# Kernel optimization log

Measured on AMD Instinct MI355X. Metric: run time of the kernel, lower is better.

The kernel has to match this reference:

```python
import jax, jax.numpy as jnp
import numpy as np

N = 100000      # nodes
E = 3200000     # edges (avg degree 32)
F_IN = 500      # input features
HID = 8         # per-head hidden dim (layer 1)
HEADS = 8       # heads (layer 1)
NC = 41         # num classes (layer 2, 1 head)


def setup_inputs() -> dict:
    key = jax.random.key(0)
    ks = jax.random.split(key, 8)
    x = jax.random.normal(ks[0], (N, F_IN), jnp.float32)
    edge_index = jax.random.randint(ks[1], (2, E), 0, N, dtype=jnp.int64)
    W1 = jax.random.normal(ks[2], (F_IN, HEADS * HID), jnp.float32) / np.sqrt(F_IN)
    a1_src = jax.random.normal(ks[3], (HEADS, HID), jnp.float32) / np.sqrt(HID)
    a1_dst = jax.random.normal(ks[4], (HEADS, HID), jnp.float32) / np.sqrt(HID)
    W2 = jax.random.normal(ks[5], (HEADS * HID, NC), jnp.float32) / np.sqrt(HEADS * HID)
    a2_src = jax.random.normal(ks[6], (1, NC), jnp.float32) / np.sqrt(NC)
    a2_dst = jax.random.normal(ks[7], (1, NC), jnp.float32) / np.sqrt(NC)
    return {"x": x, "edge_index": edge_index, "W1": W1, "a1_src": a1_src,
            "a1_dst": a1_dst, "W2": W2, "a2_src": a2_src, "a2_dst": a2_dst}


def gat_layer(x, edge_index, W, a_src, a_dst, heads, out_dim, concat):
    n = x.shape[0]
    h = (x @ W).reshape(n, heads, out_dim)                    # [N,H,D]
    # per-node attention halves (avoids gathering full features for logits)
    alpha_src = jnp.einsum('nhd,hd->nh', h, a_src)            # [N,H]
    alpha_dst = jnp.einsum('nhd,hd->nh', h, a_dst)            # [N,H]
    src, dst = edge_index[0], edge_index[1]
    e = jax.nn.leaky_relu(alpha_src[src] + alpha_dst[dst], 0.2)  # [E,H]
    # segment softmax over incoming edges of each destination node
    e_max = jax.lax.stop_gradient(jax.ops.segment_max(e, dst, num_segments=n))
    e_exp = jnp.exp(e - e_max[dst])
    denom = jax.ops.segment_sum(e_exp, dst, num_segments=n)
    alpha = e_exp / (denom[dst] + 1e-16)                      # [E,H]
    msg = alpha[:, :, None] * h[src]                          # [E,H,D]
    out = jax.ops.segment_sum(msg, dst, num_segments=n)       # [N,H,D]
    return out.reshape(n, heads * out_dim) if concat else out.mean(axis=1)


def reference(x, edge_index, W1, a1_src, a1_dst, W2, a2_src, a2_dst):
    # dropout layers are identity at inference
    h = gat_layer(x, edge_index, W1, a1_src, a1_dst, HEADS, HID, True)   # [N,64]
    h = jax.nn.elu(h)
    out = gat_layer(h, edge_index, W2, a2_src, a2_dst, 1, NC, False)     # [N,41]
    return jax.nn.log_softmax(out, axis=1)
```

## Files before the change

### kernel.cpp

```cpp
#include <hip/hip_runtime.h>
#include <hip/hip_bf16.h>
#include <math.h>


#define DEV __device__ __forceinline__

constexpr int N_NODES = 100000;
constexpr int N_EDGES = 3200000;
constexpr int F_IN    = 500;
constexpr int HEADS   = 8;
constexpr int HID     = 8;
constexpr int D1      = HEADS * HID;
constexpr int NC      = 41;
constexpr int NCP     = 64;

constexpr int NB    = 196;
constexpr int BCAP  = 20480;
constexpr int CSTR  = 16;
constexpr int SEPT  = 8;
constexpr int SCHUNK = 512 * SEPT;
constexpr int SBLKS = (N_EDGES + SCHUNK - 1) / SCHUNK;

constexpr int GROWS = 32;
constexpr int LROW  = 520;
constexpr int GBLKS = N_NODES / GROWS;

constexpr int WSTR = 68;

typedef __attribute__((ext_vector_type(8))) short bf16x8;
typedef __attribute__((ext_vector_type(4))) float f32x4;

DEV float bf2f(unsigned short u) {
    return __uint_as_float(((unsigned int)u) << 16);
}
DEV unsigned short f2b(float f) {
    unsigned int u = __float_as_uint(f);
    unsigned int r = (u + 0x7FFFu + ((u >> 16) & 1u)) >> 16;
    return (unsigned short)r;
}
DEV float leaky(float e) { return e > 0.f ? e : 0.2f * e; }
DEV float readlane_f(float v, int l) {
    return __uint_as_float((unsigned int)__builtin_amdgcn_readlane((int)__float_as_uint(v), l));
}

__global__ void k_detect(const void* xraw, const void* eraw, int* flags) {
    const int lane = threadIdx.x & 63;
    const unsigned short* xu = (const unsigned short*)xraw;
    unsigned short v = xu[2 * lane];
    int e = (v >> 7) & 0xFF;
    int valid = (e == 0 || (e >= 90 && e <= 150)) ? 1 : 0;
    unsigned long long vm = __ballot(valid);
    const unsigned int* eu = (const unsigned int*)eraw;
    unsigned long long zm = __ballot(eu[2 * lane + 1] == 0u);
    if (lane == 0) {
        flags[0] = (__popcll(vm) < 56) ? 1 : 0;
        flags[1] = (__popcll(zm) == 64) ? 1 : 0;
    }
}

__global__ __launch_bounds__(256) void k_convert(const void* w1, const void* a1s, const void* a1d,
                                                 const void* w2, const void* a2s, const void* a2d,
                                                 const int* flags,
                                                 unsigned short* W1frag, float* A1Sf, float* A1Df,
                                                 float* W2f, float* A2Sf, float* A2Df) {
    const bool f32 = flags[0] != 0;
    if (blockIdx.x == 0) {
        auto conv = [&](const void* src, float* dst, int n) {
            if (f32) {
                const float* s = (const float*)src;
                for (int i = threadIdx.x; i < n; i += blockDim.x) dst[i] = s[i];
            } else {
                const unsigned short* s = (const unsigned short*)src;
                for (int i = threadIdx.x; i < n; i += blockDim.x) dst[i] = bf2f(s[i]);
            }
        };
        conv(a1s, A1Sf, HEADS * HID);
        conv(a1d, A1Df, HEADS * HID);
        conv(w2, W2f, D1 * NC);
        conv(a2s, A2Sf, NC);
        conv(a2d, A2Df, NC);
    }
    for (int idx = blockIdx.x * 256 + threadIdx.x; idx < 4 * 16 * 64 * 8; idx += 64 * 256) {
        int wid = idx >> 13, kb = (idx >> 9) & 15, ln = (idx >> 3) & 63, j = idx & 7;
        int k = kb * 32 + (ln >> 4) * 8 + j;
        int n = wid * 16 + (ln & 15);
        unsigned short bits = 0;
        if (k < F_IN) {
            if (f32) bits = f2b(((const float*)w1)[k * D1 + n]);
            else     bits = ((const unsigned short*)w1)[k * D1 + n];
        }
        W1frag[idx] = bits;
    }
}

__global__ __launch_bounds__(512, 8) void k_gemm1_scat(const void* xraw, const void* eraw,
                                                       const int* flags,
                                                       const unsigned short* __restrict__ W1frag,
                                                       const float* A1Sf, const float* A1Df,
                                                       unsigned short* __restrict__ h1b,
                                                       float* __restrict__ as1,
                                                       float* __restrict__ ad1,
                                                       int* bucket_cnt, unsigned int* staging) {
    __shared__ unsigned short ldsx[GROWS * LROW];
    const int t = threadIdx.x;

    if (blockIdx.x < SBLKS) {
        int* bh = (int*)ldsx;
        for (int i = t; i < NB; i += 512) bh[i] = 0;
        __syncthreads();
        const bool e64 = flags[1] != 0;
        const unsigned int* eu = (const unsigned int*)eraw;
        const int e0 = blockIdx.x * SCHUNK;
        int sv[SEPT], dv[SEPT];
#pragma unroll
        for (int k = 0; k < SEPT; k++) {
            int i = e0 + k * 512 + t;
            if (i < N_EDGES) {
                if (e64) { sv[k] = (int)eu[2 * i]; dv[k] = (int)eu[2 * (N_EDGES + i)]; }
                else     { sv[k] = (int)eu[i];     dv[k] = (int)eu[N_EDGES + i]; }
                atomicAdd(&bh[dv[k] >> 9], 1);
            } else dv[k] = -1;
        }
        __syncthreads();
        for (int i = t; i < NB; i += 512) {
            int c = bh[i];
            int base = c ? atomicAdd(&bucket_cnt[i * CSTR], c) : 0;
            bh[i] = i * BCAP + base;
        }
        __syncthreads();
#pragma unroll
        for (int k = 0; k < SEPT; k++) {
            if (dv[k] >= 0) {
                int b = dv[k] >> 9;
                int slot = atomicAdd(&bh[b], 1);
                staging[slot] = (unsigned)sv[k] | ((unsigned)(dv[k] & 511) << 17);
            }
        }
        return;
    }

    const int r0 = (blockIdx.x - SBLKS) * GROWS;
    const bool xf32 = flags[0] != 0;
#pragma unroll 4
    for (int it = 0; it < 8; it++) {
        int s = it * 512 + t;
        int row = s >> 7, c4 = s & 127;
        int row_g = r0 + row;
        ushort4 v = make_ushort4(0, 0, 0, 0);
        if (c4 < 125) {
            if (xf32) {
                float4 f = *(const float4*)((const float*)xraw + (size_t)row_g * F_IN + c4 * 4);
                v = make_ushort4(f2b(f.x), f2b(f.y), f2b(f.z), f2b(f.w));
            } else {
                v = *(const ushort4*)((const unsigned short*)xraw + (size_t)row_g * F_IN + c4 * 4);
            }
        }
        *(ushort4*)(ldsx + row * LROW + c4 * 4) = v;
    }
    __syncthreads();

    const int lane = t & 63;
    const int w = t >> 6;
    const int wid = __builtin_amdgcn_readfirstlane(w & 3);
    const int mb  = __builtin_amdgcn_readfirstlane(w >> 2);
    const int m = lane & 15, q = lane >> 4;
    f32x4 acc = {0.f, 0.f, 0.f, 0.f};
    const unsigned short* wf = W1frag + (size_t)wid * 8192;
    const unsigned short* arow = ldsx + (mb * 16 + m) * LROW + q * 8;
#pragma unroll 4
    for (int kb = 0; kb < 16; kb++) {
        bf16x8 b = *(const bf16x8*)(wf + (kb * 64 + lane) * 8);
        bf16x8 a = *(const bf16x8*)(arow + kb * 32);
        acc = __builtin_amdgcn_mfma_f32_16x16x32_bf16(a, b, acc, 0, 0, 0);
    }
    const int col = wid * 16 + m;
    const float a_s = A1Sf[col], a_d = A1Df[col];
    const int h = 2 * wid + (m >> 3);
#pragma unroll
    for (int reg = 0; reg < 4; reg++) {
        int gr = r0 + mb * 16 + q * 4 + reg;
        float vacc = acc[reg];
        h1b[(size_t)gr * D1 + col] = f2b(vacc);
        float ts = vacc * a_s, td = vacc * a_d;
        ts += __shfl_xor(ts, 1, 64); td += __shfl_xor(td, 1, 64);
        ts += __shfl_xor(ts, 2, 64); td += __shfl_xor(td, 2, 64);
        ts += __shfl_xor(ts, 4, 64); td += __shfl_xor(td, 4, 64);
        if ((lane & 7) == 0) {
            as1[gr * HEADS + h] = ts;
            ad1[gr * HEADS + h] = td;
        }
    }
}

__global__ void k_cscan(const int* bucket_cnt, int* cbase, int* off) {
    __shared__ int s[256];
    int t = threadIdx.x;
    s[t] = (t < NB) ? bucket_cnt[t * CSTR] : 0;
    __syncthreads();
    for (int o = 1; o < 256; o <<= 1) {
        int v = (t >= o) ? s[t - o] : 0;
        __syncthreads();
        s[t] += v;
        __syncthreads();
    }
    if (t < NB) cbase[t + 1] = s[t];
    if (t == 0) { cbase[0] = 0; off[N_NODES] = N_EDGES; }
}

__global__ __launch_bounds__(512) void k_csr_build(const unsigned int* __restrict__ staging,
                                                   const int* __restrict__ bucket_cnt,
                                                   const int* __restrict__ cbase,
                                                   int* __restrict__ off, int* __restrict__ csr) {
    __shared__ int sdeg[512];
    __shared__ int scur[512];
    const int t = threadIdx.x;
    const int b = blockIdx.x;
    const int n0 = b << 9;
    const int start = b * BCAP;
    const int end = start + bucket_cnt[b * CSTR];
    const int base = cbase[b];
    sdeg[t] = 0;
    __syncthreads();
    for (int i = start + t; i < end; i += 512)
        atomicAdd(&sdeg[staging[i] >> 17], 1);
    __syncthreads();
    int d = sdeg[t];
    for (int o = 1; o < 512; o <<= 1) {
        int v = (t >= o) ? sdeg[t - o] : 0;
        __syncthreads();
        sdeg[t] += v;
        __syncthreads();
    }
    int excl = sdeg[t] - d;
    if (n0 + t < N_NODES) off[n0 + t] = base + excl;
    scur[t] = base + excl;
    __syncthreads();
    for (int i = start + t; i < end; i += 512) {
        unsigned v = staging[i];
        int slot = atomicAdd(&scur[v >> 17], 1);
        csr[slot] = (int)(v & 0x1FFFFu);
    }
}

__global__ __launch_bounds__(256) void k_agg1(const int* __restrict__ csr,
                                              const int* __restrict__ off,
                                              const unsigned short* __restrict__ h1b,
                                              const float* __restrict__ as1,
                                              const float* __restrict__ ad1,
                                              float* __restrict__ h1e) {
    __shared__ float wlds[4][8 * WSTR];
    const int t = threadIdx.x;
    const int lane = t & 63;
    const int n = (blockIdx.x * blockDim.x + t) >> 6;
    if (n >= N_NODES) return;
    const int beg = off[n], end = off[n + 1];
    const int h0 = lane >> 3;
    float* wl = wlds[(t >> 6) & 3];
    const float* wrow = wl + h0 * WSTR;
    const float* adp = ad1 + n * HEADS;
    float acc = 0.f, dsum = 0.f;
    for (int base = beg; base < end; base += 64) {
        const int cnt = min(64, end - base);
        int sl = 0;
        if (lane < cnt) {
            sl = csr[base + lane];
            const float* ap = as1 + sl * HEADS;
            float4 aa = *(const float4*)(ap);
            float4 ab = *(const float4*)(ap + 4);
            wl[0 * WSTR + lane] = __expf(leaky(aa.x + adp[0]));
            wl[1 * WSTR + lane] = __expf(leaky(aa.y + adp[1]));
            wl[2 * WSTR + lane] = __expf(leaky(aa.z + adp[2]));
            wl[3 * WSTR + lane] = __expf(leaky(aa.w + adp[3]));
            wl[4 * WSTR + lane] = __expf(leaky(ab.x + adp[4]));
            wl[5 * WSTR + lane] = __expf(leaky(ab.y + adp[5]));
            wl[6 * WSTR + lane] = __expf(leaky(ab.z + adp[6]));
            wl[7 * WSTR + lane] = __expf(leaky(ab.w + adp[7]));
        }
        asm volatile("s_waitcnt lgkmcnt(0)" ::: "memory");
        int j = 0;
        for (; j + 4 <= cnt; j += 4) {
            int s0 = __builtin_amdgcn_readlane(sl, j);
            int s1 = __builtin_amdgcn_readlane(sl, j + 1);
            int s2 = __builtin_amdgcn_readlane(sl, j + 2);
            int s3 = __builtin_amdgcn_readlane(sl, j + 3);
            float4 wv = *(const float4*)(wrow + j);
            float g0 = bf2f(h1b[(size_t)s0 * D1 + lane]);
            float g1 = bf2f(h1b[(size_t)s1 * D1 + lane]);
            float g2 = bf2f(h1b[(size_t)s2 * D1 + lane]);
            float g3 = bf2f(h1b[(size_t)s3 * D1 + lane]);
            acc = fmaf(wv.x, g0, acc); dsum += wv.x;
            acc = fmaf(wv.y, g1, acc); dsum += wv.y;
            acc = fmaf(wv.z, g2, acc); dsum += wv.z;
            acc = fmaf(wv.w, g3, acc); dsum += wv.w;
        }
        for (; j < cnt; j++) {
            int s = __builtin_amdgcn_readlane(sl, j);
            float w = wrow[j];
            acc = fmaf(w, bf2f(h1b[(size_t)s * D1 + lane]), acc);
            dsum += w;
        }
    }
    float v = acc / (dsum + 1e-16f);
    float o = v > 0.f ? v : (__expf(v) - 1.f);
    h1e[(size_t)n * D1 + lane] = o;
}

__global__ __launch_bounds__(256) void k_gemm2(const float* __restrict__ h1e,
                                               const float* __restrict__ W2f,
                                               const float* __restrict__ A2Sf,
                                               const float* __restrict__ A2Df,
                                               unsigned short* __restrict__ h2p,
                                               float* __restrict__ as2,
                                               float* __restrict__ ad2) {
    const int row = blockIdx.x * blockDim.x + threadIdx.x;
    if (row >= N_NODES) return;
    float acc[NC];
#pragma unroll
    for (int c = 0; c < NC; c++) acc[c] = 0.f;
    const float* xr = h1e + (size_t)row * D1;
    for (int k = 0; k < D1; k += 4) {
        float4 hv = *(const float4*)(xr + k);
#pragma unroll
        for (int c = 0; c < NC; c++) {
            acc[c] = fmaf(hv.x, W2f[(k + 0) * NC + c], acc[c]);
            acc[c] = fmaf(hv.y, W2f[(k + 1) * NC + c], acc[c]);
            acc[c] = fmaf(hv.z, W2f[(k + 2) * NC + c], acc[c]);
            acc[c] = fmaf(hv.w, W2f[(k + 3) * NC + c], acc[c]);
        }
    }
    float ts = 0.f, td = 0.f;
#pragma unroll
    for (int c = 0; c < NC; c++) {
        h2p[(size_t)row * NCP + c] = f2b(acc[c]);
        ts = fmaf(acc[c], A2Sf[c], ts);
        td = fmaf(acc[c], A2Df[c], td);
    }
    as2[row] = ts;
    ad2[row] = td;
}

__global__ __launch_bounds__(256) void k_agg2(const int* __restrict__ csr,
                                              const int* __restrict__ off,
                                              const unsigned short* __restrict__ h2p,
                                              const float* __restrict__ as2,
                                              const float* __restrict__ ad2,
                                              const int* flags, void* out) {
    const int lane = threadIdx.x & 63;
    const int n = (blockIdx.x * blockDim.x + threadIdx.x) >> 6;
    if (n >= N_NODES) return;
    const int beg = off[n], end = off[n + 1];
    const float ad = ad2[n];
    const bool act = lane < NC;
    const int cl = act ? lane : 0;
    float acc = 0.f, dsum = 0.f;
    for (int base = beg; base < end; base += 64) {
        const int cnt = min(64, end - base);
        int idx = min(base + lane, N_EDGES - 1);
        int sl = csr[idx];
        float w = __expf(leaky(as2[sl] + ad));
        int j = 0;
        for (; j + 4 <= cnt; j += 4) {
            int s0 = __builtin_amdgcn_readlane(sl, j);
            int s1 = __builtin_amdgcn_readlane(sl, j + 1);
            int s2 = __builtin_amdgcn_readlane(sl, j + 2);
            int s3 = __builtin_amdgcn_readlane(sl, j + 3);
            float w0 = readlane_f(w, j);
            float w1 = readlane_f(w, j + 1);
            float w2 = readlane_f(w, j + 2);
            float w3 = readlane_f(w, j + 3);
            float g0 = bf2f(h2p[(size_t)s0 * NCP + cl]);
            float g1 = bf2f(h2p[(size_t)s1 * NCP + cl]);
            float g2 = bf2f(h2p[(size_t)s2 * NCP + cl]);
            float g3 = bf2f(h2p[(size_t)s3 * NCP + cl]);
            acc = fmaf(w0, g0, acc); dsum += w0;
            acc = fmaf(w1, g1, acc); dsum += w1;
            acc = fmaf(w2, g2, acc); dsum += w2;
            acc = fmaf(w3, g3, acc); dsum += w3;
        }
        for (; j < cnt; j++) {
            int s = __builtin_amdgcn_readlane(sl, j);
            float wj = readlane_f(w, j);
            acc = fmaf(wj, bf2f(h2p[(size_t)s * NCP + cl]), acc);
            dsum += wj;
        }
    }
    float val = acc / (dsum + 1e-16f);
    float v = act ? val : -INFINITY;
    float m = v;
#pragma unroll
    for (int o = 1; o < 64; o <<= 1) m = fmaxf(m, __shfl_xor(m, o, 64));
    float ex = act ? __expf(val - m) : 0.f;
#pragma unroll
    for (int o = 1; o < 64; o <<= 1) ex += __shfl_xor(ex, o, 64);
    float res = val - m - __logf(ex);
    if (act) {
        if (flags[0])
            ((float*)out)[(size_t)n * NC + lane] = res;
        else
            ((__hip_bfloat16*)out)[(size_t)n * NC + lane] = __float2bfloat16(res);
    }
}

extern "C" void kernel_launch(void* const* d_in, const int* in_sizes, int n_in,
                              void* d_out, int out_size, void* d_ws, size_t ws_size,
                              hipStream_t stream) {
    char* p = (char*)d_ws;
    auto alloc = [&](size_t bytes) -> void* {
        void* r = (void*)p;
        p += (bytes + 255) & ~(size_t)255;
        return r;
    };
    int* flags  = (int*)alloc(16);
    unsigned short* W1frag = (unsigned short*)alloc(4 * 16 * 64 * 8 * 2);
    float* A1Sf = (float*)alloc(HEADS * HID * 4);
    float* A1Df = (float*)alloc(HEADS * HID * 4);
    float* W2f  = (float*)alloc((size_t)D1 * NC * 4);
    float* A2Sf = (float*)alloc(NC * 4);
    float* A2Df = (float*)alloc(NC * 4);
    unsigned short* h1b = (unsigned short*)alloc((size_t)N_NODES * D1 * 2);
    float* as1  = (float*)alloc((size_t)N_NODES * HEADS * 4);
    float* ad1  = (float*)alloc((size_t)N_NODES * HEADS * 4);
    float* h1e  = (float*)alloc((size_t)N_NODES * D1 * 4);
    unsigned short* h2p = (unsigned short*)alloc((size_t)N_NODES * NCP * 2);
    float* as2  = (float*)alloc((size_t)N_NODES * 4);
    float* ad2  = (float*)alloc((size_t)N_NODES * 4);
    int* off    = (int*)alloc((size_t)(N_NODES + 1) * 4);
    int* csr    = (int*)alloc((size_t)N_EDGES * 4);
    int* bucket_cnt = (int*)alloc((size_t)NB * CSTR * 4);
    int* cbase      = (int*)alloc((size_t)(NB + 1) * 4);
    unsigned int* staging = (unsigned int*)h1e;

    hipMemsetAsync(bucket_cnt, 0, (size_t)NB * CSTR * 4, stream);

    k_detect<<<1, 64, 0, stream>>>(d_in[0], d_in[1], flags);
    k_convert<<<64, 256, 0, stream>>>(d_in[2], d_in[3], d_in[4], d_in[5], d_in[6], d_in[7],
                                      flags, W1frag, A1Sf, A1Df, W2f, A2Sf, A2Df);
    k_gemm1_scat<<<SBLKS + GBLKS, 512, 0, stream>>>(d_in[0], d_in[1], flags, W1frag,
                                                    A1Sf, A1Df, h1b, as1, ad1,
                                                    bucket_cnt, staging);
    k_cscan<<<1, 256, 0, stream>>>(bucket_cnt, cbase, off);
    k_csr_build<<<NB, 512, 0, stream>>>(staging, bucket_cnt, cbase, off, csr);

    k_agg1<<<25000, 256, 0, stream>>>(csr, off, h1b, as1, ad1, h1e);
    k_gemm2<<<391, 256, 0, stream>>>(h1e, W2f, A2Sf, A2Df, h2p, as2, ad2);
    k_agg2<<<25000, 256, 0, stream>>>(csr, off, h2p, as2, ad2, flags, d_out);
}
```

Baseline: 605.0 us.

## Locally sort edge scatter in LDS for coalesced staging writes; widen CSR build blocks

```diff
diff --git a/kernel.cpp b/kernel.cpp
--- a/kernel.cpp
+++ b/kernel.cpp
@@ -105,12 +105,20 @@
     const int t = threadIdx.x;
 
     if (blockIdx.x < SBLKS) {
-        int* bh = (int*)ldsx;
-        for (int i = t; i < NB; i += 512) bh[i] = 0;
-        __syncthreads();
+        int* hist  = (int*)ldsx;
+        int* lbase = hist + 256;
+        int* gbase = lbase + 256;
+        unsigned char* pbk = (unsigned char*)(gbase + 196);
+        unsigned* pay = (unsigned*)(pbk + 4096);
+
         const bool e64 = flags[1] != 0;
         const unsigned int* eu = (const unsigned int*)eraw;
         const int e0 = blockIdx.x * SCHUNK;
+        const int total = min(SCHUNK, N_EDGES - e0);
+
+        for (int i = t; i < 256; i += 512) hist[i] = 0;
+        __syncthreads();
+
         int sv[SEPT], dv[SEPT];
 #pragma unroll
         for (int k = 0; k < SEPT; k++) {
@@ -118,23 +126,45 @@
             if (i < N_EDGES) {
                 if (e64) { sv[k] = (int)eu[2 * i]; dv[k] = (int)eu[2 * (N_EDGES + i)]; }
                 else     { sv[k] = (int)eu[i];     dv[k] = (int)eu[N_EDGES + i]; }
-                atomicAdd(&bh[dv[k] >> 9], 1);
+                atomicAdd(&hist[dv[k] >> 9], 1);
             } else dv[k] = -1;
         }
         __syncthreads();
-        for (int i = t; i < NB; i += 512) {
-            int c = bh[i];
-            int base = c ? atomicAdd(&bucket_cnt[i * CSTR], c) : 0;
-            bh[i] = i * BCAP + base;
-        }
-        __syncthreads();
+
+        if (t < 256) lbase[t] = hist[t];
+        __syncthreads();
+        for (int o = 1; o < 256; o <<= 1) {
+            int v = 0;
+            if (t < 256 && t >= o) v = lbase[t - o];
+            __syncthreads();
+            if (t < 256) lbase[t] += v;
+            __syncthreads();
+        }
+        if (t < NB) {
+            int c = hist[t];
+            int ex = lbase[t] - c;
+            int base = c ? atomicAdd(&bucket_cnt[t * CSTR], c) : 0;
+            lbase[t] = ex;
+            gbase[t] = t * BCAP + base;
+        }
+        __syncthreads();
+        if (t < NB) hist[t] = lbase[t];
+        __syncthreads();
+
 #pragma unroll
         for (int k = 0; k < SEPT; k++) {
             if (dv[k] >= 0) {
                 int b = dv[k] >> 9;
-                int slot = atomicAdd(&bh[b], 1);
-                staging[slot] = (unsigned)sv[k] | ((unsigned)(dv[k] & 511) << 17);
+                int slot = atomicAdd(&hist[b], 1);
+                pay[slot] = (unsigned)sv[k] | ((unsigned)(dv[k] & 511) << 17);
+                pbk[slot] = (unsigned char)b;
             }
+        }
+        __syncthreads();
+
+        for (int j = t; j < total; j += 512) {
+            int b = pbk[j];
+            staging[gbase[b] + (j - lbase[b])] = pay[j];
         }
         return;
     }
@@ -207,10 +237,10 @@
     if (t == 0) { cbase[0] = 0; off[N_NODES] = N_EDGES; }
 }
 
-__global__ __launch_bounds__(512) void k_csr_build(const unsigned int* __restrict__ staging,
-                                                   const int* __restrict__ bucket_cnt,
-                                                   const int* __restrict__ cbase,
-                                                   int* __restrict__ off, int* __restrict__ csr) {
+__global__ __launch_bounds__(1024) void k_csr_build(const unsigned int* __restrict__ staging,
+                                                    const int* __restrict__ bucket_cnt,
+                                                    const int* __restrict__ cbase,
+                                                    int* __restrict__ off, int* __restrict__ csr) {
     __shared__ int sdeg[512];
     __shared__ int scur[512];
     const int t = threadIdx.x;
@@ -219,23 +249,25 @@
     const int start = b * BCAP;
     const int end = start + bucket_cnt[b * CSTR];
     const int base = cbase[b];
-    sdeg[t] = 0;
+    if (t < 512) sdeg[t] = 0;
     __syncthreads();
-    for (int i = start + t; i < end; i += 512)
+    for (int i = start + t; i < end; i += 1024)
         atomicAdd(&sdeg[staging[i] >> 17], 1);
     __syncthreads();
-    int d = sdeg[t];
+    int d = (t < 512) ? sdeg[t] : 0;
     for (int o = 1; o < 512; o <<= 1) {
-        int v = (t >= o) ? sdeg[t - o] : 0;
-        __syncthreads();
-        sdeg[t] += v;
-        __syncthreads();
-    }
-    int excl = sdeg[t] - d;
-    if (n0 + t < N_NODES) off[n0 + t] = base + excl;
-    scur[t] = base + excl;
+        int v = (t < 512 && t >= o) ? sdeg[t - o] : 0;
+        __syncthreads();
+        if (t < 512) sdeg[t] += v;
+        __syncthreads();
+    }
+    if (t < 512) {
+        int excl = sdeg[t] - d;
+        if (n0 + t < N_NODES) off[n0 + t] = base + excl;
+        scur[t] = base + excl;
+    }
     __syncthreads();
-    for (int i = start + t; i < end; i += 512) {
+    for (int i = start + t; i < end; i += 1024) {
         unsigned v = staging[i];
         int slot = atomicAdd(&scur[v >> 17], 1);
         csr[slot] = (int)(v & 0x1FFFFu);
@@ -439,7 +471,7 @@
                                                     A1Sf, A1Df, h1b, as1, ad1,
                                                     bucket_cnt, staging);
     k_cscan<<<1, 256, 0, stream>>>(bucket_cnt, cbase, off);
-    k_csr_build<<<NB, 512, 0, stream>>>(staging, bucket_cnt, cbase, off, csr);
+    k_csr_build<<<NB, 1024, 0, stream>>>(staging, bucket_cnt, cbase, off, csr);
 
     k_agg1<<<25000, 256, 0, stream>>>(csr, off, h1b, as1, ad1, h1e);
     k_gemm2<<<391, 256, 0, stream>>>(h1e, W2f, A2Sf, A2Df, h2p, as2, ad2);
```

Result: no change. 593.3 us (-1.9%).
